# Performance work log

Hardware: AMD Instinct MI355X
Metric: run time of the kernel (lower is better)

The kernel has to match this reference:

```python
import jax, jax.numpy as jnp
import numpy as np

H, D = 8, 16
HD = H * D
SCALE0 = float(1.0 / np.sqrt(D * 1))   # degree-0 dot-product scale (order m=1)
SCALE1 = float(1.0 / np.sqrt(D * 3))   # degree-1 dot-product scale (order m=3)
SHARED = float(np.sqrt(0.5))           # shared_scale = sqrt(1/2) for DOT_PROD + SHARED
NEG = -1e9


def _split_heads_q(x):  # (b,n,HD,m) -> (b,H,n,D,m)
    b, n, _, m = x.shape
    return x.reshape(b, n, H, D, m).transpose(0, 2, 1, 3, 4)


def _split_heads_k(x):  # (b,n,N,HD,m) -> (b,H,n,N,D,m)
    b, n, N, _, m = x.shape
    return x.reshape(b, n, N, H, D, m).transpose(0, 3, 1, 2, 4, 5)


def _augment_kv(k, v, feats, W_self, null_k, null_v):
    # attend_self: VNLinear self key/value; use_null_kv: learned null tokens.
    b, n = feats.shape[:2]
    m = feats.shape[-1]
    skv = jnp.einsum('oc,bncm->bnom', W_self, feats)          # (b,n,2HD,m)
    sk, sv = jnp.split(skv, 2, axis=-2)
    sk = _split_heads_q(sk)[:, :, :, None]                     # (b,H,n,1,D,m)
    sv = _split_heads_q(sv)[:, :, :, None]
    nk = jnp.broadcast_to(null_k[None, :, None, None], (b, H, n, 1, D, m))
    nv = jnp.broadcast_to(null_v[None, :, None, None], (b, H, n, 1, D, m))
    k = jnp.concatenate([nk, sk, k], axis=3)                   # (b,H,n,2+N,D,m)
    v = jnp.concatenate([nv, sv, v], axis=3)
    return k, v


def _merge_heads(x):  # (b,H,n,D,m) -> (b,n,HD,m)
    b, _, n, _, m = x.shape
    return x.transpose(0, 2, 1, 3, 4).reshape(b, n, HD, m)


def _forward(q0, k0, v0, q1, k1, v1, feats0, feats1, edges,
             W_self_kv0, W_self_kv1, W_bias, self_bias, null_bias,
             null_k0, null_v0, null_k1, null_v1, head_weights1,
             W_out0, W_out1, neighbor_mask):
    b, n, N = edges.shape[:3]
    q0h, k0h, v0h = _split_heads_q(q0), _split_heads_k(k0), _split_heads_k(v0)
    q1h, k1h, v1h = _split_heads_q(q1), _split_heads_k(k1), _split_heads_k(v1)
    k0h, v0h = _augment_kv(k0h, v0h, feats0, W_self_kv0, null_k0, null_v0)
    k1h, v1h = _augment_kv(k1h, v1h, feats1, W_self_kv1, null_k1, null_v1)

    # pair bias for degree 0 (to_order==1); prepend null/self bias columns
    edge_bias = jnp.einsum('bnje,he->bhnj', edges, W_bias)     # (b,H,n,N)
    nb = jnp.broadcast_to(null_bias[None, :, None, None], (b, H, n, 1))
    sb = jnp.broadcast_to(self_bias[None, :, None, None], (b, H, n, 1))
    bias = jnp.concatenate([nb, sb, edge_bias], axis=-1)        # (b,H,n,2+N)

    sim0 = jnp.einsum('bhndm,bhnjdm->bhnj', q0h, k0h) * SCALE0 + bias
    w1 = jax.nn.softplus(head_weights1)                         # (1,H,1,1)
    sim1 = jnp.einsum('bhndm,bhnjdm->bhnj', q1h, k1h) * (SCALE1 * w1)

    total = (sim0 + sim1) * SHARED
    mask = jnp.concatenate(
        [jnp.ones((b, 1, n, 2), dtype=bool),                    # null + self always valid
         neighbor_mask[:, None]], axis=-1)
    total = jnp.where(mask, total, NEG)
    attn = jax.nn.softmax(total, axis=-1)                       # shared across degrees

    out0 = _merge_heads(jnp.einsum('bhnj,bhnjdm->bhndm', attn, v0h))
    out1 = _merge_heads(jnp.einsum('bhnj,bhnjdm->bhndm', attn, v1h))

    y0 = jnp.einsum('oc,bncm->bnom', W_out0, out0)              # FiberLinear deg 0
    y1 = jnp.einsum('oc,bncm->bnom', W_out1, out1)              # FiberLinear deg 1
    return y0, y1


def setup_inputs() -> dict:
    key = jax.random.key(0)
    ks = jax.random.split(key, 20)
    b, n, N, e = 1, 2048, 32, 32
    d0, d1 = 128, 64
    f = lambda k, s: jax.random.normal(k, s, dtype=jnp.float32) * 0.1
    return {
        'q0': f(ks[0], (b, n, HD, 1)), 'k0': f(ks[1], (b, n, N, HD, 1)), 'v0': f(ks[2], (b, n, N, HD, 1)),
        'q1': f(ks[3], (b, n, HD, 3)), 'k1': f(ks[4], (b, n, N, HD, 3)), 'v1': f(ks[5], (b, n, N, HD, 3)),
        'feats0': f(ks[6], (b, n, d0, 1)), 'feats1': f(ks[7], (b, n, d1, 3)),
        'edges': f(ks[8], (b, n, N, e)),
        'W_self_kv0': f(ks[9], (2 * HD, d0)), 'W_self_kv1': f(ks[10], (2 * HD, d1)),
        'W_bias': f(ks[11], (H, e)),
        'self_bias': jnp.zeros((H,), jnp.float32), 'null_bias': jnp.zeros((H,), jnp.float32),
        'null_k0': jnp.zeros((H, D, 1), jnp.float32), 'null_v0': jnp.zeros((H, D, 1), jnp.float32),
        'null_k1': jnp.zeros((H, D, 3), jnp.float32), 'null_v1': jnp.zeros((H, D, 3), jnp.float32),
        'head_weights1': jnp.full((1, H, 1, 1), float(np.log(np.e - 1.0)), jnp.float32),
        'W_out0': f(ks[12], (d0, HD)), 'W_out1': f(ks[13], (d1, HD)),
        'neighbor_mask': jax.random.uniform(ks[14], (b, n, N)) > 0.1,
    }


def reference(q0, k0, v0, q1, k1, v1, feats0, feats1, edges,
              W_self_kv0, W_self_kv1, W_bias, self_bias, null_bias,
              null_k0, null_v0, null_k1, null_v1, head_weights1,
              W_out0, W_out1, neighbor_mask):
    return _forward(q0, k0, v0, q1, k1, v1, feats0, feats1, edges,
                    W_self_kv0, W_self_kv1, W_bias, self_bias, null_bias,
                    null_k0, null_v0, null_k1, null_v1, head_weights1,
                    W_out0, W_out1, neighbor_mask)
```

## Files before the change

### kernel.cpp

```cpp
#include <hip/hip_runtime.h>

constexpr int kH  = 8;
constexpr int kD  = 16;
constexpr int kHD = 128;
constexpr int kN  = 32;
constexpr int kE  = 32;
constexpr int kD0 = 128;
constexpr int kD1 = 64;
constexpr int kP  = 4;
constexpr int kP3 = 2;

constexpr float SCALE0   = 0.25f;
constexpr float SCALE1   = 0.14433756729740643f;
constexpr float SHARED_S = 0.70710678118654752f;
constexpr float NEGV     = -1e9f;


__global__ __launch_bounds__(256) void k1_selfkv(
    const float* __restrict__ q0, const float* __restrict__ q1,
    const float* __restrict__ feats0, const float* __restrict__ feats1,
    const float* __restrict__ Wskv0, const float* __restrict__ Wskv1,
    const float* __restrict__ self_bias, const float* __restrict__ null_bias,
    const float* __restrict__ nk0, const float* __restrict__ nk1,
    const float* __restrict__ hw1,
    float* __restrict__ ws_sc, float* __restrict__ ws_sv0, float* __restrict__ ws_sv1)
{
  const int i0 = blockIdx.x * kP;
  const int t  = threadIdx.x;
  __shared__ __align__(16) float f0s[kP][kD0];
  __shared__ __align__(16) float f1s[kP][kD1 * 3];
  __shared__ __align__(16) float q0s[kP][kHD];
  __shared__ __align__(16) float q1s[kP][kHD * 3];
  __shared__ float sk0L[kP][kHD];
  __shared__ float sk1L[kP][kHD * 3];
  __shared__ float w1s[kH];

  for (int u = t; u < kP * 32; u += 256) { int p = u >> 5, r = u & 31;
    ((float4*)f0s[p])[r] = ((const float4*)(feats0 + (size_t)(i0 + p) * kD0))[r]; }
  for (int u = t; u < kP * 48; u += 256) { int p = u / 48, r = u % 48;
    ((float4*)f1s[p])[r] = ((const float4*)(feats1 + (size_t)(i0 + p) * kD1 * 3))[r]; }
  for (int u = t; u < kP * 32; u += 256) { int p = u >> 5, r = u & 31;
    ((float4*)q0s[p])[r] = ((const float4*)(q0 + (size_t)(i0 + p) * kHD))[r]; }
  for (int u = t; u < kP * 96; u += 256) { int p = u / 96, r = u % 96;
    ((float4*)q1s[p])[r] = ((const float4*)(q1 + (size_t)(i0 + p) * kHD * 3))[r]; }
  if (t < kH) w1s[t] = log1pf(expf(hw1[t]));
  __syncthreads();

  float acc0[kP] = {};
  {
    const float4* wr = (const float4*)(Wskv0 + t * kD0);
    #pragma unroll
    for (int g = 0; g < 32; ++g) {
      float4 w = wr[g]; int c = g * 4;
      #pragma unroll
      for (int p = 0; p < kP; ++p)
        acc0[p] += w.x * f0s[p][c] + w.y * f0s[p][c + 1]
                 + w.z * f0s[p][c + 2] + w.w * f0s[p][c + 3];
    }
  }
  float acc1[kP][3] = {};
  {
    const float4* wr = (const float4*)(Wskv1 + t * kD1);
    #pragma unroll
    for (int g = 0; g < 16; ++g) {
      float4 w = wr[g]; int c = g * 4;
      float wv[4] = {w.x, w.y, w.z, w.w};
      #pragma unroll
      for (int q = 0; q < 4; ++q) {
        #pragma unroll
        for (int p = 0; p < kP; ++p) {
          const float* fp = &f1s[p][(c + q) * 3];
          acc1[p][0] += wv[q] * fp[0];
          acc1[p][1] += wv[q] * fp[1];
          acc1[p][2] += wv[q] * fp[2];
        }
      }
    }
  }
  if (t < kHD) {
    #pragma unroll
    for (int p = 0; p < kP; ++p) {
      sk0L[p][t] = acc0[p];
      sk1L[p][t * 3 + 0] = acc1[p][0];
      sk1L[p][t * 3 + 1] = acc1[p][1];
      sk1L[p][t * 3 + 2] = acc1[p][2];
    }
  } else {
    const int o = t - kHD;
    #pragma unroll
    for (int p = 0; p < kP; ++p) {
      ws_sv0[(size_t)(i0 + p) * kHD + o] = acc0[p];
      float* sp = ws_sv1 + (size_t)(i0 + p) * kHD * 3 + o * 3;
      sp[0] = acc1[p][0]; sp[1] = acc1[p][1]; sp[2] = acc1[p][2];
    }
  }
  __syncthreads();

  if (t < kP * 16) {
    const int p = t >> 4, idx = t & 15;
    const int h = idx & 7;
    const bool is_self = idx >= 8;
    float s0 = 0.f, s1 = 0.f, bias;
    if (is_self) {
      #pragma unroll
      for (int d = 0; d < kD; ++d) s0 += q0s[p][h * kD + d] * sk0L[p][h * kD + d];
      #pragma unroll
      for (int x = 0; x < 48; ++x) s1 += q1s[p][h * 48 + x] * sk1L[p][h * 48 + x];
      bias = self_bias[h];
    } else {
      #pragma unroll
      for (int d = 0; d < kD; ++d) s0 += q0s[p][h * kD + d] * nk0[h * kD + d];
      #pragma unroll
      for (int x = 0; x < 48; ++x) s1 += q1s[p][h * 48 + x] * nk1[h * 48 + x];
      bias = null_bias[h];
    }
    float total = (s0 * SCALE0 + bias + s1 * SCALE1 * w1s[h]) * SHARED_S;
    ws_sc[(size_t)(i0 + p) * 272 + h * 34 + (is_self ? 1 : 0)] = total;
  }
}

__global__ __launch_bounds__(256) void k2_sims(
    const float* __restrict__ q0, const float* __restrict__ q1,
    const float* __restrict__ k0, const float* __restrict__ k1,
    const float* __restrict__ edges, const float* __restrict__ Wbias,
    const float* __restrict__ hw1, const int* __restrict__ nmask,
    float* __restrict__ ws_sc)
{
  const int i0 = blockIdx.x * kP;
  const int t  = threadIdx.x;
  __shared__ float q0s[kP][kH * 17];
  __shared__ float q1s[kP][kH * 49];
  __shared__ float edg[kP][kN * 33];
  __shared__ float wbT[kE * kH];
  __shared__ float w1s[kH];
  __shared__ __align__(16) float scL[kP][272];

  for (int u = t; u < kP * 32; u += 256) { int p = u >> 5, r = u & 31;
    float4 v = ((const float4*)(q0 + (size_t)(i0 + p) * kHD))[r];
    int c = r * 4, h = c >> 4, d = c & 15;
    float* dst = &q0s[p][h * 17 + d];
    dst[0] = v.x; dst[1] = v.y; dst[2] = v.z; dst[3] = v.w; }
  for (int u = t; u < kP * 96; u += 256) { int p = u / 96, r = u % 96;
    float4 v = ((const float4*)(q1 + (size_t)(i0 + p) * kHD * 3))[r];
    int c = r * 4, h = c / 48, x = c % 48;
    float* dst = &q1s[p][h * 49 + x];
    dst[0] = v.x; dst[1] = v.y; dst[2] = v.z; dst[3] = v.w; }
  for (int u = t; u < kP * 256; u += 256) { int p = u >> 8, r = u & 255;
    float4 v = ((const float4*)(edges + (size_t)(i0 + p) * kN * kE))[r];
    int j = r >> 3, e4 = (r & 7) * 4;
    float* dst = &edg[p][j * 33 + e4];
    dst[0] = v.x; dst[1] = v.y; dst[2] = v.z; dst[3] = v.w; }
  if (t < kH * kE) { int h = t >> 5, e = t & 31; wbT[e * 8 + h] = Wbias[t]; }
  if (t < kH) w1s[t] = log1pf(expf(hw1[t]));
  if (t < kP * 16) { int p = t >> 4, idx = t & 15, h = idx & 7, slot = idx >> 3;
    scL[p][h * 34 + slot] = ws_sc[(size_t)(i0 + p) * 272 + h * 34 + slot]; }
  __syncthreads();

  {
    const int j = t >> 3, h = t & 7;
    #pragma unroll
    for (int p = 0; p < kP; ++p) {
      const int i = i0 + p;
      float bias = 0.f;
      #pragma unroll
      for (int e = 0; e < kE; ++e) bias += edg[p][j * 33 + e] * wbT[e * 8 + h];
      float s0 = 0.f;
      const float4* kr0 = (const float4*)(k0 + (size_t)(i * kN + j) * kHD + h * kD);
      #pragma unroll
      for (int g = 0; g < 4; ++g) {
        float4 w = kr0[g]; int x = h * 17 + g * 4;
        s0 += w.x * q0s[p][x] + w.y * q0s[p][x + 1]
            + w.z * q0s[p][x + 2] + w.w * q0s[p][x + 3];
      }
      float s1 = 0.f;
      const float4* kr1 = (const float4*)(k1 + (size_t)(i * kN + j) * kHD * 3 + h * 48);
      #pragma unroll
      for (int g = 0; g < 12; ++g) {
        float4 w = kr1[g]; int x = h * 49 + g * 4;
        s1 += w.x * q1s[p][x] + w.y * q1s[p][x + 1]
            + w.z * q1s[p][x + 2] + w.w * q1s[p][x + 3];
      }
      float total = (s0 * SCALE0 + bias + s1 * SCALE1 * w1s[h]) * SHARED_S;
      bool valid = nmask[(size_t)i * kN + j] != 0;
      scL[p][h * 34 + 2 + j] = valid ? total : NEGV;
    }
  }
  __syncthreads();

  if (t < kP * kH) {
    const int p = t >> 3, h = t & 7;
    float* row = &scL[p][h * 34];
    float mx = -1e30f;
    #pragma unroll
    for (int u = 0; u < 34; ++u) mx = fmaxf(mx, row[u]);
    float sum = 0.f;
    #pragma unroll
    for (int u = 0; u < 34; ++u) sum += __expf(row[u] - mx);
    float inv = 1.f / sum;
    #pragma unroll
    for (int u = 0; u < 34; ++u) row[u] = __expf(row[u] - mx) * inv;
  }
  __syncthreads();

  for (int u = t; u < kP * 68; u += 256) {
    int p = u / 68, r = u % 68;
    ((float4*)(ws_sc + (size_t)(i0 + p) * 272))[r] = ((float4*)scL[p])[r];
  }
}

__global__ __launch_bounds__(256) void k3_out(
    const float* __restrict__ v0, const float* __restrict__ v1,
    const float* __restrict__ nv0, const float* __restrict__ nv1,
    const float* __restrict__ ws_sc,
    const float* __restrict__ ws_sv0, const float* __restrict__ ws_sv1,
    const float* __restrict__ Wout0, const float* __restrict__ Wout1,
    float* __restrict__ out, int n_total)
{
  const int i0 = blockIdx.x * kP3;
  const int t  = threadIdx.x;
  __shared__ __align__(16) float attnL[kP3][272];
  __shared__ __align__(16) float o0L[kP3][kHD];
  __shared__ __align__(16) float o1L[kP3][kHD * 3];

  if (t < kP3 * 68) {
    int p = t / 68, r = t % 68;
    ((float4*)attnL[p])[r] = ((const float4*)(ws_sc + (size_t)(i0 + p) * 272))[r];
  }
  __syncthreads();

  {
    const int p = t >> 7, i = i0 + p;
    const int s = t & 127;
    float4 acc;
    if (s < 32) {
      const int h = s >> 2;
      const float* at = attnL[p] + h * 34;
      float4 nv = ((const float4*)nv0)[s];
      float4 sv = ((const float4*)(ws_sv0 + (size_t)i * kHD))[s];
      acc.x = at[0] * nv.x + at[1] * sv.x;
      acc.y = at[0] * nv.y + at[1] * sv.y;
      acc.z = at[0] * nv.z + at[1] * sv.z;
      acc.w = at[0] * nv.w + at[1] * sv.w;
      const float4* vp = (const float4*)(v0 + (size_t)i * kN * kHD) + s;
      float4 vbuf[8];
      #pragma unroll
      for (int g = 0; g < 4; ++g) {
        #pragma unroll
        for (int r = 0; r < 8; ++r) vbuf[r] = vp[(g * 8 + r) * 32];
        #pragma unroll
        for (int r = 0; r < 8; ++r) {
          float a = at[2 + g * 8 + r];
          acc.x += a * vbuf[r].x; acc.y += a * vbuf[r].y;
          acc.z += a * vbuf[r].z; acc.w += a * vbuf[r].w;
        }
      }
      ((float4*)o0L[p])[s] = acc;
    } else {
      const int s1 = s - 32;
      const int h = s1 / 12;
      const float* at = attnL[p] + h * 34;
      float4 nv = ((const float4*)nv1)[s1];
      float4 sv = ((const float4*)(ws_sv1 + (size_t)i * kHD * 3))[s1];
      acc.x = at[0] * nv.x + at[1] * sv.x;
      acc.y = at[0] * nv.y + at[1] * sv.y;
      acc.z = at[0] * nv.z + at[1] * sv.z;
      acc.w = at[0] * nv.w + at[1] * sv.w;
      const float4* vp = (const float4*)(v1 + (size_t)i * kN * kHD * 3) + s1;
      float4 vbuf[8];
      #pragma unroll
      for (int g = 0; g < 4; ++g) {
        #pragma unroll
        for (int r = 0; r < 8; ++r) vbuf[r] = vp[(g * 8 + r) * 96];
        #pragma unroll
        for (int r = 0; r < 8; ++r) {
          float a = at[2 + g * 8 + r];
          acc.x += a * vbuf[r].x; acc.y += a * vbuf[r].y;
          acc.z += a * vbuf[r].z; acc.w += a * vbuf[r].w;
        }
      }
      ((float4*)o1L[p])[s1] = acc;
    }
  }
  __syncthreads();

  for (int u = t; u < 320; u += 256) {
    if (u < 128) {
      float acc[kP3] = {};
      const float4* wr = (const float4*)(Wout0 + u * kHD);
      #pragma unroll
      for (int g = 0; g < 32; ++g) {
        float4 w = wr[g]; int c = g * 4;
        #pragma unroll
        for (int p = 0; p < kP3; ++p)
          acc[p] += w.x * o0L[p][c] + w.y * o0L[p][c + 1]
                  + w.z * o0L[p][c + 2] + w.w * o0L[p][c + 3];
      }
      #pragma unroll
      for (int p = 0; p < kP3; ++p) out[(size_t)(i0 + p) * kHD + u] = acc[p];
    } else {
      const int v2 = u - 128, o = v2 / 3, m = v2 - o * 3;
      float acc[kP3] = {};
      const float4* wr = (const float4*)(Wout1 + o * kHD);
      #pragma unroll
      for (int g = 0; g < 32; ++g) {
        float4 w = wr[g]; int c = g * 4;
        #pragma unroll
        for (int p = 0; p < kP3; ++p)
          acc[p] += w.x * o1L[p][(c + 0) * 3 + m] + w.y * o1L[p][(c + 1) * 3 + m]
                  + w.z * o1L[p][(c + 2) * 3 + m] + w.w * o1L[p][(c + 3) * 3 + m];
      }
      #pragma unroll
      for (int p = 0; p < kP3; ++p)
        out[(size_t)n_total * kHD + (size_t)(i0 + p) * 192 + v2] = acc[p];
    }
  }
}

extern "C" void kernel_launch(void* const* d_in, const int* in_sizes, int n_in,
                              void* d_out, int out_size, void* d_ws, size_t ws_size,
                              hipStream_t stream) {
  const int n = in_sizes[0] / kHD;
  const float* q0     = (const float*)d_in[0];
  const float* k0     = (const float*)d_in[1];
  const float* v0     = (const float*)d_in[2];
  const float* q1     = (const float*)d_in[3];
  const float* k1     = (const float*)d_in[4];
  const float* v1     = (const float*)d_in[5];
  const float* feats0 = (const float*)d_in[6];
  const float* feats1 = (const float*)d_in[7];
  const float* edges  = (const float*)d_in[8];
  const float* Wskv0  = (const float*)d_in[9];
  const float* Wskv1  = (const float*)d_in[10];
  const float* Wbias  = (const float*)d_in[11];
  const float* sbias  = (const float*)d_in[12];
  const float* nbias  = (const float*)d_in[13];
  const float* nk0    = (const float*)d_in[14];
  const float* nv0    = (const float*)d_in[15];
  const float* nk1    = (const float*)d_in[16];
  const float* nv1    = (const float*)d_in[17];
  const float* hw1    = (const float*)d_in[18];
  const float* Wout0  = (const float*)d_in[19];
  const float* Wout1  = (const float*)d_in[20];
  const int*   nmask  = (const int*)d_in[21];

  float* ws     = (float*)d_ws;
  float* ws_sc  = ws;
  float* ws_sv0 = ws + (size_t)n * 272;
  float* ws_sv1 = ws + (size_t)n * 272 + (size_t)n * 128;

  k1_selfkv<<<n / kP, 256, 0, stream>>>(q0, q1, feats0, feats1, Wskv0, Wskv1,
                                        sbias, nbias, nk0, nk1, hw1,
                                        ws_sc, ws_sv0, ws_sv1);
  k2_sims<<<n / kP, 256, 0, stream>>>(q0, q1, k0, k1, edges, Wbias, hw1, nmask, ws_sc);
  k3_out<<<n / kP3, 256, 0, stream>>>(v0, v1, nv0, nv1, ws_sc, ws_sv0, ws_sv1,
                                      Wout0, Wout1, (float*)d_out, n);
}
```

Before: 372.3 us.

## Split output stage into accumulation kernel and batched projection kernel

The fused attention-accumulate plus output-projection kernel is split in two. The accumulation kernel writes the per-node attended values back into the self-value workspace buffers in place, with a launch-bounds occupancy hint. A new projection kernel loads eight nodes per block so each Wout row is reused across more nodes, replacing the previous two-node reuse. This adds a kernel launch and a round trip of the intermediate through global memory, and it underuses threads in the projection stage.

```diff
diff --git a/kernel.cpp b/kernel.cpp
--- a/kernel.cpp
+++ b/kernel.cpp
@@ -9,6 +9,7 @@
 constexpr int kD1 = 64;
 constexpr int kP  = 4;
 constexpr int kP3 = 2;
+constexpr int kPP = 8;
 
 constexpr float SCALE0   = 0.25f;
 constexpr float SCALE1   = 0.14433756729740643f;
@@ -208,19 +209,15 @@
   }
 }
 
-__global__ __launch_bounds__(256) void k3_out(
+__global__ __launch_bounds__(256, 4) void k3_accum(
     const float* __restrict__ v0, const float* __restrict__ v1,
     const float* __restrict__ nv0, const float* __restrict__ nv1,
     const float* __restrict__ ws_sc,
-    const float* __restrict__ ws_sv0, const float* __restrict__ ws_sv1,
-    const float* __restrict__ Wout0, const float* __restrict__ Wout1,
-    float* __restrict__ out, int n_total)
+    float* __restrict__ ws_sv0, float* __restrict__ ws_sv1)
 {
   const int i0 = blockIdx.x * kP3;
   const int t  = threadIdx.x;
   __shared__ __align__(16) float attnL[kP3][272];
-  __shared__ __align__(16) float o0L[kP3][kHD];
-  __shared__ __align__(16) float o1L[kP3][kHD * 3];
 
   if (t < kP3 * 68) {
     int p = t / 68, r = t % 68;
@@ -228,91 +225,103 @@
   }
   __syncthreads();
 
-  {
-    const int p = t >> 7, i = i0 + p;
-    const int s = t & 127;
-    float4 acc;
-    if (s < 32) {
-      const int h = s >> 2;
-      const float* at = attnL[p] + h * 34;
-      float4 nv = ((const float4*)nv0)[s];
-      float4 sv = ((const float4*)(ws_sv0 + (size_t)i * kHD))[s];
-      acc.x = at[0] * nv.x + at[1] * sv.x;
-      acc.y = at[0] * nv.y + at[1] * sv.y;
-      acc.z = at[0] * nv.z + at[1] * sv.z;
-      acc.w = at[0] * nv.w + at[1] * sv.w;
-      const float4* vp = (const float4*)(v0 + (size_t)i * kN * kHD) + s;
-      float4 vbuf[8];
-      #pragma unroll
-      for (int g = 0; g < 4; ++g) {
-        #pragma unroll
-        for (int r = 0; r < 8; ++r) vbuf[r] = vp[(g * 8 + r) * 32];
-        #pragma unroll
-        for (int r = 0; r < 8; ++r) {
-          float a = at[2 + g * 8 + r];
-          acc.x += a * vbuf[r].x; acc.y += a * vbuf[r].y;
-          acc.z += a * vbuf[r].z; acc.w += a * vbuf[r].w;
-        }
-      }
-      ((float4*)o0L[p])[s] = acc;
-    } else {
-      const int s1 = s - 32;
-      const int h = s1 / 12;
-      const float* at = attnL[p] + h * 34;
-      float4 nv = ((const float4*)nv1)[s1];
-      float4 sv = ((const float4*)(ws_sv1 + (size_t)i * kHD * 3))[s1];
-      acc.x = at[0] * nv.x + at[1] * sv.x;
-      acc.y = at[0] * nv.y + at[1] * sv.y;
-      acc.z = at[0] * nv.z + at[1] * sv.z;
-      acc.w = at[0] * nv.w + at[1] * sv.w;
-      const float4* vp = (const float4*)(v1 + (size_t)i * kN * kHD * 3) + s1;
-      float4 vbuf[8];
-      #pragma unroll
-      for (int g = 0; g < 4; ++g) {
-        #pragma unroll
-        for (int r = 0; r < 8; ++r) vbuf[r] = vp[(g * 8 + r) * 96];
-        #pragma unroll
-        for (int r = 0; r < 8; ++r) {
-          float a = at[2 + g * 8 + r];
-          acc.x += a * vbuf[r].x; acc.y += a * vbuf[r].y;
-          acc.z += a * vbuf[r].z; acc.w += a * vbuf[r].w;
-        }
-      }
-      ((float4*)o1L[p])[s1] = acc;
-    }
-  }
-  __syncthreads();
-
-  for (int u = t; u < 320; u += 256) {
-    if (u < 128) {
-      float acc[kP3] = {};
-      const float4* wr = (const float4*)(Wout0 + u * kHD);
-      #pragma unroll
-      for (int g = 0; g < 32; ++g) {
-        float4 w = wr[g]; int c = g * 4;
-        #pragma unroll
-        for (int p = 0; p < kP3; ++p)
-          acc[p] += w.x * o0L[p][c] + w.y * o0L[p][c + 1]
-                  + w.z * o0L[p][c + 2] + w.w * o0L[p][c + 3];
-      }
-      #pragma unroll
-      for (int p = 0; p < kP3; ++p) out[(size_t)(i0 + p) * kHD + u] = acc[p];
-    } else {
-      const int v2 = u - 128, o = v2 / 3, m = v2 - o * 3;
-      float acc[kP3] = {};
-      const float4* wr = (const float4*)(Wout1 + o * kHD);
-      #pragma unroll
-      for (int g = 0; g < 32; ++g) {
-        float4 w = wr[g]; int c = g * 4;
-        #pragma unroll
-        for (int p = 0; p < kP3; ++p)
-          acc[p] += w.x * o1L[p][(c + 0) * 3 + m] + w.y * o1L[p][(c + 1) * 3 + m]
-                  + w.z * o1L[p][(c + 2) * 3 + m] + w.w * o1L[p][(c + 3) * 3 + m];
-      }
-      #pragma unroll
-      for (int p = 0; p < kP3; ++p)
-        out[(size_t)n_total * kHD + (size_t)(i0 + p) * 192 + v2] = acc[p];
-    }
+  const int p = t >> 7, i = i0 + p;
+  const int s = t & 127;
+  float4 acc;
+  if (s < 32) {
+    const int h = s >> 2;
+    const float* at = attnL[p] + h * 34;
+    float4 nv = ((const float4*)nv0)[s];
+    float4 sv = ((const float4*)(ws_sv0 + (size_t)i * kHD))[s];
+    acc.x = at[0] * nv.x + at[1] * sv.x;
+    acc.y = at[0] * nv.y + at[1] * sv.y;
+    acc.z = at[0] * nv.z + at[1] * sv.z;
+    acc.w = at[0] * nv.w + at[1] * sv.w;
+    const float4* vp = (const float4*)(v0 + (size_t)i * kN * kHD) + s;
+    float4 vbuf[8];
+    #pragma unroll
+    for (int g = 0; g < 4; ++g) {
+      #pragma unroll
+      for (int r = 0; r < 8; ++r) vbuf[r] = vp[(g * 8 + r) * 32];
+      #pragma unroll
+      for (int r = 0; r < 8; ++r) {
+        float a = at[2 + g * 8 + r];
+        acc.x += a * vbuf[r].x; acc.y += a * vbuf[r].y;
+        acc.z += a * vbuf[r].z; acc.w += a * vbuf[r].w;
+      }
+    }
+    ((float4*)(ws_sv0 + (size_t)i * kHD))[s] = acc;
+  } else {
+    const int s1 = s - 32;
+    const int h = s1 / 12;
+    const float* at = attnL[p] + h * 34;
+    float4 nv = ((const float4*)nv1)[s1];
+    float4 sv = ((const float4*)(ws_sv1 + (size_t)i * kHD * 3))[s1];
+    acc.x = at[0] * nv.x + at[1] * sv.x;
+    acc.y = at[0] * nv.y + at[1] * sv.y;
+    acc.z = at[0] * nv.z + at[1] * sv.z;
+    acc.w = at[0] * nv.w + at[1] * sv.w;
+    const float4* vp = (const float4*)(v1 + (size_t)i * kN * kHD * 3) + s1;
+    float4 vbuf[8];
+    #pragma unroll
+    for (int g = 0; g < 4; ++g) {
+      #pragma unroll
+      for (int r = 0; r < 8; ++r) vbuf[r] = vp[(g * 8 + r) * 96];
+      #pragma unroll
+      for (int r = 0; r < 8; ++r) {
+        float a = at[2 + g * 8 + r];
+        acc.x += a * vbuf[r].x; acc.y += a * vbuf[r].y;
+        acc.z += a * vbuf[r].z; acc.w += a * vbuf[r].w;
+      }
+    }
+    ((float4*)(ws_sv1 + (size_t)i * kHD * 3))[s1] = acc;
+  }
+}
+
+__global__ __launch_bounds__(320) void k4_proj(
+    const float* __restrict__ ws_o0, const float* __restrict__ ws_o1,
+    const float* __restrict__ Wout0, const float* __restrict__ Wout1,
+    float* __restrict__ out, int n_total)
+{
+  const int i0 = blockIdx.x * kPP;
+  const int t  = threadIdx.x;
+  __shared__ __align__(16) float o0L[kPP][kHD];
+  __shared__ __align__(16) float o1L[kPP][kHD * 3];
+
+  for (int u = t; u < kPP * 32; u += 320) { int p = u >> 5, r = u & 31;
+    ((float4*)o0L[p])[r] = ((const float4*)(ws_o0 + (size_t)(i0 + p) * kHD))[r]; }
+  for (int u = t; u < kPP * 96; u += 320) { int p = u / 96, r = u % 96;
+    ((float4*)o1L[p])[r] = ((const float4*)(ws_o1 + (size_t)(i0 + p) * kHD * 3))[r]; }
+  __syncthreads();
+
+  if (t < 128) {
+    float acc[kPP] = {};
+    const float4* wr = (const float4*)(Wout0 + t * kHD);
+    #pragma unroll
+    for (int g = 0; g < 32; ++g) {
+      float4 w = wr[g]; int c = g * 4;
+      #pragma unroll
+      for (int p = 0; p < kPP; ++p)
+        acc[p] += w.x * o0L[p][c] + w.y * o0L[p][c + 1]
+                + w.z * o0L[p][c + 2] + w.w * o0L[p][c + 3];
+    }
+    #pragma unroll
+    for (int p = 0; p < kPP; ++p) out[(size_t)(i0 + p) * kHD + t] = acc[p];
+  } else {
+    const int v2 = t - 128, o = v2 / 3, m = v2 - o * 3;
+    float acc[kPP] = {};
+    const float4* wr = (const float4*)(Wout1 + o * kHD);
+    #pragma unroll
+    for (int g = 0; g < 32; ++g) {
+      float4 w = wr[g]; int c = g * 4;
+      #pragma unroll
+      for (int p = 0; p < kPP; ++p)
+        acc[p] += w.x * o1L[p][(c + 0) * 3 + m] + w.y * o1L[p][(c + 1) * 3 + m]
+                + w.z * o1L[p][(c + 2) * 3 + m] + w.w * o1L[p][(c + 3) * 3 + m];
+    }
+    #pragma unroll
+    for (int p = 0; p < kPP; ++p)
+      out[(size_t)n_total * kHD + (size_t)(i0 + p) * 192 + v2] = acc[p];
   }
 }
 
@@ -352,6 +361,6 @@
                                         sbias, nbias, nk0, nk1, hw1,
                                         ws_sc, ws_sv0, ws_sv1);
   k2_sims<<<n / kP, 256, 0, stream>>>(q0, q1, k0, k1, edges, Wbias, hw1, nmask, ws_sc);
-  k3_out<<<n / kP3, 256, 0, stream>>>(v0, v1, nv0, nv1, ws_sc, ws_sv0, ws_sv1,
-                                      Wout0, Wout1, (float*)d_out, n);
-}
+  k3_accum<<<n / kP3, 256, 0, stream>>>(v0, v1, nv0, nv1, ws_sc, ws_sv0, ws_sv1);
+  k4_proj<<<n / kPP, 320, 0, stream>>>(ws_sv0, ws_sv1, Wout0, Wout1, (float*)d_out, n);
+}
```

Measured after the change: 360.5 us. 1.03x faster.

## Fuse self-KV, similarity, softmax and output kernels into one kernel

Applied to the files above, without the earlier changes.

Merges the three kernels into a single kernel that processes two positions per block. Self key/value projections, scores and attention weights now stay in shared memory instead of going through a workspace. The GEMV-style loops are split across quads of lanes and combined with shuffle reductions, and the per-row softmax uses 16-lane shuffles. This removes two launches and the workspace round trips, but weight matrices are now re-read per two positions rather than four, and shared-memory use per block rises.

```diff
diff --git a/kernel.cpp b/kernel.cpp
--- a/kernel.cpp
+++ b/kernel.cpp
@@ -7,224 +7,230 @@
 constexpr int kE  = 32;
 constexpr int kD0 = 128;
 constexpr int kD1 = 64;
-constexpr int kP  = 4;
-constexpr int kP3 = 2;
+constexpr int kPos = 2;
 
 constexpr float SCALE0   = 0.25f;
 constexpr float SCALE1   = 0.14433756729740643f;
 constexpr float SHARED_S = 0.70710678118654752f;
 constexpr float NEGV     = -1e9f;
 
-
-__global__ __launch_bounds__(256) void k1_selfkv(
+__global__ __launch_bounds__(256, 4) void se3_fused(
     const float* __restrict__ q0, const float* __restrict__ q1,
+    const float* __restrict__ k0, const float* __restrict__ k1,
+    const float* __restrict__ v0, const float* __restrict__ v1,
     const float* __restrict__ feats0, const float* __restrict__ feats1,
+    const float* __restrict__ edges,
     const float* __restrict__ Wskv0, const float* __restrict__ Wskv1,
-    const float* __restrict__ self_bias, const float* __restrict__ null_bias,
+    const float* __restrict__ Wbias,
+    const float* __restrict__ sbias, const float* __restrict__ nbias,
     const float* __restrict__ nk0, const float* __restrict__ nk1,
+    const float* __restrict__ nv0, const float* __restrict__ nv1,
     const float* __restrict__ hw1,
-    float* __restrict__ ws_sc, float* __restrict__ ws_sv0, float* __restrict__ ws_sv1)
+    const float* __restrict__ Wout0, const float* __restrict__ Wout1,
+    const int* __restrict__ nmask,
+    float* __restrict__ out, int n_total)
 {
-  const int i0 = blockIdx.x * kP;
+  const int i0 = blockIdx.x * kPos;
   const int t  = threadIdx.x;
-  __shared__ __align__(16) float f0s[kP][kD0];
-  __shared__ __align__(16) float f1s[kP][kD1 * 3];
-  __shared__ __align__(16) float q0s[kP][kHD];
-  __shared__ __align__(16) float q1s[kP][kHD * 3];
-  __shared__ float sk0L[kP][kHD];
-  __shared__ float sk1L[kP][kHD * 3];
+
+  __shared__ __align__(16) float f0s[kPos][kD0];
+  __shared__ __align__(16) float f1s[kPos][kD1 * 3];
+  __shared__ __align__(16) float q0s[kPos][kHD];
+  __shared__ __align__(16) float q1s[kPos][kHD * 3];
+  __shared__ float edg[kPos][kN * (kE + 1)];
+  __shared__ float wbs[kH * kE];
   __shared__ float w1s[kH];
-
-  for (int u = t; u < kP * 32; u += 256) { int p = u >> 5, r = u & 31;
+  __shared__ int   nmL[kPos][kN];
+  __shared__ float sk0[kPos][kHD];
+  __shared__ __align__(16) float sk1[kPos][kHD * 3];
+  __shared__ __align__(16) float sv0[kPos][kHD];
+  __shared__ __align__(16) float sv1[kPos][kHD * 3];
+  __shared__ float sc[kPos][kH][36];
+  __shared__ __align__(16) float o0[kPos][kHD];
+  __shared__ __align__(16) float o1[kPos][kHD * 3];
+
+  if (t < kPos * 32) { int p = t >> 5, r = t & 31;
     ((float4*)f0s[p])[r] = ((const float4*)(feats0 + (size_t)(i0 + p) * kD0))[r]; }
-  for (int u = t; u < kP * 48; u += 256) { int p = u / 48, r = u % 48;
+  else if (t < kPos * 32 + kPos * 48) { int u = t - kPos * 32, p = u / 48, r = u % 48;
     ((float4*)f1s[p])[r] = ((const float4*)(feats1 + (size_t)(i0 + p) * kD1 * 3))[r]; }
-  for (int u = t; u < kP * 32; u += 256) { int p = u >> 5, r = u & 31;
+  if (t >= 160 && t < 160 + kPos * 32) { int u = t - 160, p = u >> 5, r = u & 31;
     ((float4*)q0s[p])[r] = ((const float4*)(q0 + (size_t)(i0 + p) * kHD))[r]; }
-  for (int u = t; u < kP * 96; u += 256) { int p = u / 96, r = u % 96;
-    ((float4*)q1s[p])[r] = ((const float4*)(q1 + (size_t)(i0 + p) * kHD * 3))[r]; }
+  {
+    int u = t; if (u < kPos * 96) { int p = u / 96, r = u % 96;
+      ((float4*)q1s[p])[r] = ((const float4*)(q1 + (size_t)(i0 + p) * kHD * 3))[r]; }
+  }
+  for (int u = t; u < kPos * 256; u += 256) { int p = u >> 8, r = u & 255;
+    float4 v = ((const float4*)(edges + (size_t)(i0 + p) * kN * kE))[r];
+    int j = r >> 3, e4 = (r & 7) * 4;
+    float* dst = &edg[p][j * 33 + e4];
+    dst[0] = v.x; dst[1] = v.y; dst[2] = v.z; dst[3] = v.w; }
+  if (t < kH * kE) wbs[t] = Wbias[t];
   if (t < kH) w1s[t] = log1pf(expf(hw1[t]));
-  __syncthreads();
-
-  float acc0[kP] = {};
-  {
-    const float4* wr = (const float4*)(Wskv0 + t * kD0);
-    #pragma unroll
-    for (int g = 0; g < 32; ++g) {
-      float4 w = wr[g]; int c = g * 4;
-      #pragma unroll
-      for (int p = 0; p < kP; ++p)
-        acc0[p] += w.x * f0s[p][c] + w.y * f0s[p][c + 1]
-                 + w.z * f0s[p][c + 2] + w.w * f0s[p][c + 3];
-    }
-  }
-  float acc1[kP][3] = {};
-  {
-    const float4* wr = (const float4*)(Wskv1 + t * kD1);
-    #pragma unroll
-    for (int g = 0; g < 16; ++g) {
-      float4 w = wr[g]; int c = g * 4;
+  if (t < kPos * kN) { int p = t >> 5, j = t & 31;
+    nmL[p][j] = nmask[(size_t)(i0 + p) * kN + j]; }
+  __syncthreads();
+
+  const int q4 = t & 3;
+  const int qg = t >> 2;
+
+  #pragma unroll
+  for (int pass = 0; pass < 4; ++pass) {
+    const int r = qg + 64 * pass;
+    const float4* w0r = (const float4*)(Wskv0 + (size_t)r * kD0);
+    float a0[kPos] = {};
+    #pragma unroll
+    for (int g = 0; g < 8; ++g) {
+      float4 w = w0r[q4 + 4 * g]; int c = (q4 + 4 * g) * 4;
+      #pragma unroll
+      for (int p = 0; p < kPos; ++p)
+        a0[p] += w.x * f0s[p][c] + w.y * f0s[p][c + 1]
+               + w.z * f0s[p][c + 2] + w.w * f0s[p][c + 3];
+    }
+    const float4* w1r = (const float4*)(Wskv1 + (size_t)r * kD1);
+    float a1[kPos][3] = {};
+    #pragma unroll
+    for (int g = 0; g < 4; ++g) {
+      float4 w = w1r[q4 + 4 * g]; int c = (q4 + 4 * g) * 4;
       float wv[4] = {w.x, w.y, w.z, w.w};
       #pragma unroll
-      for (int q = 0; q < 4; ++q) {
-        #pragma unroll
-        for (int p = 0; p < kP; ++p) {
-          const float* fp = &f1s[p][(c + q) * 3];
-          acc1[p][0] += wv[q] * fp[0];
-          acc1[p][1] += wv[q] * fp[1];
-          acc1[p][2] += wv[q] * fp[2];
-        }
-      }
-    }
-  }
-  if (t < kHD) {
-    #pragma unroll
-    for (int p = 0; p < kP; ++p) {
-      sk0L[p][t] = acc0[p];
-      sk1L[p][t * 3 + 0] = acc1[p][0];
-      sk1L[p][t * 3 + 1] = acc1[p][1];
-      sk1L[p][t * 3 + 2] = acc1[p][2];
-    }
-  } else {
-    const int o = t - kHD;
-    #pragma unroll
-    for (int p = 0; p < kP; ++p) {
-      ws_sv0[(size_t)(i0 + p) * kHD + o] = acc0[p];
-      float* sp = ws_sv1 + (size_t)(i0 + p) * kHD * 3 + o * 3;
-      sp[0] = acc1[p][0]; sp[1] = acc1[p][1]; sp[2] = acc1[p][2];
-    }
-  }
-  __syncthreads();
-
-  if (t < kP * 16) {
+      for (int k = 0; k < 4; ++k) {
+        #pragma unroll
+        for (int p = 0; p < kPos; ++p) {
+          const float* fp = &f1s[p][(c + k) * 3];
+          a1[p][0] += wv[k] * fp[0];
+          a1[p][1] += wv[k] * fp[1];
+          a1[p][2] += wv[k] * fp[2];
+        }
+      }
+    }
+    #pragma unroll
+    for (int p = 0; p < kPos; ++p) {
+      a0[p] += __shfl_xor(a0[p], 1); a0[p] += __shfl_xor(a0[p], 2);
+      #pragma unroll
+      for (int c = 0; c < 3; ++c) {
+        a1[p][c] += __shfl_xor(a1[p][c], 1);
+        a1[p][c] += __shfl_xor(a1[p][c], 2);
+      }
+    }
+    if (q4 == 0) {
+      if (r < kHD) {
+        #pragma unroll
+        for (int p = 0; p < kPos; ++p) {
+          sk0[p][r] = a0[p];
+          sk1[p][r * 3 + 0] = a1[p][0];
+          sk1[p][r * 3 + 1] = a1[p][1];
+          sk1[p][r * 3 + 2] = a1[p][2];
+        }
+      } else {
+        const int o = r - kHD;
+        #pragma unroll
+        for (int p = 0; p < kPos; ++p) {
+          sv0[p][o] = a0[p];
+          sv1[p][o * 3 + 0] = a1[p][0];
+          sv1[p][o * 3 + 1] = a1[p][1];
+          sv1[p][o * 3 + 2] = a1[p][2];
+        }
+      }
+    }
+  }
+  __syncthreads();
+
+  if (t < kPos * 16) {
     const int p = t >> 4, idx = t & 15;
     const int h = idx & 7;
     const bool is_self = idx >= 8;
     float s0 = 0.f, s1 = 0.f, bias;
     if (is_self) {
       #pragma unroll
-      for (int d = 0; d < kD; ++d) s0 += q0s[p][h * kD + d] * sk0L[p][h * kD + d];
-      #pragma unroll
-      for (int x = 0; x < 48; ++x) s1 += q1s[p][h * 48 + x] * sk1L[p][h * 48 + x];
-      bias = self_bias[h];
+      for (int d = 0; d < kD; ++d) s0 += q0s[p][h * kD + d] * sk0[p][h * kD + d];
+      #pragma unroll
+      for (int x = 0; x < 48; ++x) s1 += q1s[p][h * 48 + x] * sk1[p][h * 48 + x];
+      bias = sbias[h];
     } else {
       #pragma unroll
       for (int d = 0; d < kD; ++d) s0 += q0s[p][h * kD + d] * nk0[h * kD + d];
       #pragma unroll
       for (int x = 0; x < 48; ++x) s1 += q1s[p][h * 48 + x] * nk1[h * 48 + x];
-      bias = null_bias[h];
-    }
-    float total = (s0 * SCALE0 + bias + s1 * SCALE1 * w1s[h]) * SHARED_S;
-    ws_sc[(size_t)(i0 + p) * 272 + h * 34 + (is_self ? 1 : 0)] = total;
-  }
-}
-
-__global__ __launch_bounds__(256) void k2_sims(
-    const float* __restrict__ q0, const float* __restrict__ q1,
-    const float* __restrict__ k0, const float* __restrict__ k1,
-    const float* __restrict__ edges, const float* __restrict__ Wbias,
-    const float* __restrict__ hw1, const int* __restrict__ nmask,
-    float* __restrict__ ws_sc)
-{
-  const int i0 = blockIdx.x * kP;
-  const int t  = threadIdx.x;
-  __shared__ float q0s[kP][kH * 17];
-  __shared__ float q1s[kP][kH * 49];
-  __shared__ float edg[kP][kN * 33];
-  __shared__ float wbT[kE * kH];
-  __shared__ float w1s[kH];
-  __shared__ __align__(16) float scL[kP][272];
-
-  for (int u = t; u < kP * 32; u += 256) { int p = u >> 5, r = u & 31;
-    float4 v = ((const float4*)(q0 + (size_t)(i0 + p) * kHD))[r];
-    int c = r * 4, h = c >> 4, d = c & 15;
-    float* dst = &q0s[p][h * 17 + d];
-    dst[0] = v.x; dst[1] = v.y; dst[2] = v.z; dst[3] = v.w; }
-  for (int u = t; u < kP * 96; u += 256) { int p = u / 96, r = u % 96;
-    float4 v = ((const float4*)(q1 + (size_t)(i0 + p) * kHD * 3))[r];
-    int c = r * 4, h = c / 48, x = c % 48;
-    float* dst = &q1s[p][h * 49 + x];
-    dst[0] = v.x; dst[1] = v.y; dst[2] = v.z; dst[3] = v.w; }
-  for (int u = t; u < kP * 256; u += 256) { int p = u >> 8, r = u & 255;
-    float4 v = ((const float4*)(edges + (size_t)(i0 + p) * kN * kE))[r];
-    int j = r >> 3, e4 = (r & 7) * 4;
-    float* dst = &edg[p][j * 33 + e4];
-    dst[0] = v.x; dst[1] = v.y; dst[2] = v.z; dst[3] = v.w; }
-  if (t < kH * kE) { int h = t >> 5, e = t & 31; wbT[e * 8 + h] = Wbias[t]; }
-  if (t < kH) w1s[t] = log1pf(expf(hw1[t]));
-  if (t < kP * 16) { int p = t >> 4, idx = t & 15, h = idx & 7, slot = idx >> 3;
-    scL[p][h * 34 + slot] = ws_sc[(size_t)(i0 + p) * 272 + h * 34 + slot]; }
-  __syncthreads();
+      bias = nbias[h];
+    }
+    sc[p][h][is_self ? 1 : 0] =
+        (s0 * SCALE0 + bias + s1 * SCALE1 * w1s[h]) * SHARED_S;
+  }
 
   {
-    const int j = t >> 3, h = t & 7;
-    #pragma unroll
-    for (int p = 0; p < kP; ++p) {
+    const int h  = qg & 7;
+    const int jl = qg >> 3;
+    const float w1h = w1s[h];
+    float wbf[8];
+    #pragma unroll
+    for (int e = 0; e < 8; ++e) wbf[e] = wbs[h * kE + q4 * 8 + e];
+
+    #pragma unroll
+    for (int p = 0; p < kPos; ++p) {
       const int i = i0 + p;
-      float bias = 0.f;
-      #pragma unroll
-      for (int e = 0; e < kE; ++e) bias += edg[p][j * 33 + e] * wbT[e * 8 + h];
-      float s0 = 0.f;
-      const float4* kr0 = (const float4*)(k0 + (size_t)(i * kN + j) * kHD + h * kD);
-      #pragma unroll
-      for (int g = 0; g < 4; ++g) {
-        float4 w = kr0[g]; int x = h * 17 + g * 4;
-        s0 += w.x * q0s[p][x] + w.y * q0s[p][x + 1]
-            + w.z * q0s[p][x + 2] + w.w * q0s[p][x + 3];
-      }
-      float s1 = 0.f;
-      const float4* kr1 = (const float4*)(k1 + (size_t)(i * kN + j) * kHD * 3 + h * 48);
-      #pragma unroll
-      for (int g = 0; g < 12; ++g) {
-        float4 w = kr1[g]; int x = h * 49 + g * 4;
-        s1 += w.x * q1s[p][x] + w.y * q1s[p][x + 1]
-            + w.z * q1s[p][x + 2] + w.w * q1s[p][x + 3];
-      }
-      float total = (s0 * SCALE0 + bias + s1 * SCALE1 * w1s[h]) * SHARED_S;
-      bool valid = nmask[(size_t)i * kN + j] != 0;
-      scL[p][h * 34 + 2 + j] = valid ? total : NEGV;
-    }
-  }
-  __syncthreads();
-
-  if (t < kP * kH) {
-    const int p = t >> 3, h = t & 7;
-    float* row = &scL[p][h * 34];
-    float mx = -1e30f;
-    #pragma unroll
-    for (int u = 0; u < 34; ++u) mx = fmaxf(mx, row[u]);
-    float sum = 0.f;
-    #pragma unroll
-    for (int u = 0; u < 34; ++u) sum += __expf(row[u] - mx);
-    float inv = 1.f / sum;
-    #pragma unroll
-    for (int u = 0; u < 34; ++u) row[u] = __expf(row[u] - mx) * inv;
-  }
-  __syncthreads();
-
-  for (int u = t; u < kP * 68; u += 256) {
-    int p = u / 68, r = u % 68;
-    ((float4*)(ws_sc + (size_t)(i0 + p) * 272))[r] = ((float4*)scL[p])[r];
-  }
-}
-
-__global__ __launch_bounds__(256) void k3_out(
-    const float* __restrict__ v0, const float* __restrict__ v1,
-    const float* __restrict__ nv0, const float* __restrict__ nv1,
-    const float* __restrict__ ws_sc,
-    const float* __restrict__ ws_sv0, const float* __restrict__ ws_sv1,
-    const float* __restrict__ Wout0, const float* __restrict__ Wout1,
-    float* __restrict__ out, int n_total)
-{
-  const int i0 = blockIdx.x * kP3;
-  const int t  = threadIdx.x;
-  __shared__ __align__(16) float attnL[kP3][272];
-  __shared__ __align__(16) float o0L[kP3][kHD];
-  __shared__ __align__(16) float o1L[kP3][kHD * 3];
-
-  if (t < kP3 * 68) {
-    int p = t / 68, r = t % 68;
-    ((float4*)attnL[p])[r] = ((const float4*)(ws_sc + (size_t)(i0 + p) * 272))[r];
+      const float4 q0f = *((const float4*)(q0s[p] + h * kD) + q4);
+      float4 q1f[3];
+      #pragma unroll
+      for (int pc = 0; pc < 3; ++pc)
+        q1f[pc] = *((const float4*)(q1s[p] + h * 48 + pc * 16) + q4);
+
+      const float* k0base = k0 + (size_t)i * kN * kHD + h * kD + q4 * 4;
+      const float* k1base = k1 + (size_t)i * kN * kHD * 3 + h * 48 + q4 * 4;
+
+      float4 kv0[4];
+      float4 kv1[4][3];
+      #pragma unroll
+      for (int pp = 0; pp < 4; ++pp) {
+        const int j = pp * 8 + jl;
+        kv0[pp] = *((const float4*)(k0base + (size_t)j * kHD));
+        #pragma unroll
+        for (int pc = 0; pc < 3; ++pc)
+          kv1[pp][pc] = *((const float4*)(k1base + (size_t)j * kHD * 3 + pc * 16));
+      }
+
+      #pragma unroll
+      for (int pp = 0; pp < 4; ++pp) {
+        const int j = pp * 8 + jl;
+        float s0 = kv0[pp].x * q0f.x + kv0[pp].y * q0f.y
+                 + kv0[pp].z * q0f.z + kv0[pp].w * q0f.w;
+        float s1 = 0.f;
+        #pragma unroll
+        for (int pc = 0; pc < 3; ++pc)
+          s1 += kv1[pp][pc].x * q1f[pc].x + kv1[pp][pc].y * q1f[pc].y
+              + kv1[pp][pc].z * q1f[pc].z + kv1[pp][pc].w * q1f[pc].w;
+        float bias = 0.f;
+        #pragma unroll
+        for (int e = 0; e < 8; ++e) bias += edg[p][j * 33 + q4 * 8 + e] * wbf[e];
+
+        float part = s0 * SCALE0 + bias + s1 * SCALE1 * w1h;
+        part += __shfl_xor(part, 1);
+        part += __shfl_xor(part, 2);
+        if (q4 == 0) sc[p][h][2 + j] = nmL[p][j] ? part * SHARED_S : NEGV;
+      }
+    }
+  }
+  __syncthreads();
+
+  {
+    const int row = t >> 4;
+    const int p = row >> 3, h = row & 7, l = t & 15;
+    float* rp = sc[p][h];
+    float va = rp[2 + l], vb = rp[2 + l + 16];
+    float mx = fmaxf(va, vb);
+    #pragma unroll
+    for (int off = 8; off > 0; off >>= 1) mx = fmaxf(mx, __shfl_xor(mx, off));
+    float e0v = rp[0], e1v = rp[1];
+    mx = fmaxf(mx, fmaxf(e0v, e1v));
+    float ea = __expf(va - mx), eb = __expf(vb - mx);
+    float sum = ea + eb;
+    #pragma unroll
+    for (int off = 8; off > 0; off >>= 1) sum += __shfl_xor(sum, off);
+    float ee0 = __expf(e0v - mx), ee1 = __expf(e1v - mx);
+    float inv = 1.f / (sum + ee0 + ee1);
+    rp[2 + l] = ea * inv;
+    rp[2 + l + 16] = eb * inv;
+    if (l == 0) rp[0] = ee0 * inv;
+    if (l == 1) rp[1] = ee1 * inv;
   }
   __syncthreads();
 
@@ -234,9 +240,9 @@
     float4 acc;
     if (s < 32) {
       const int h = s >> 2;
-      const float* at = attnL[p] + h * 34;
+      const float* at = sc[p][h];
       float4 nv = ((const float4*)nv0)[s];
-      float4 sv = ((const float4*)(ws_sv0 + (size_t)i * kHD))[s];
+      float4 sv = ((const float4*)sv0[p])[s];
       acc.x = at[0] * nv.x + at[1] * sv.x;
       acc.y = at[0] * nv.y + at[1] * sv.y;
       acc.z = at[0] * nv.z + at[1] * sv.z;
@@ -254,13 +260,13 @@
           acc.z += a * vbuf[r].z; acc.w += a * vbuf[r].w;
         }
       }
-      ((float4*)o0L[p])[s] = acc;
+      ((float4*)o0[p])[s] = acc;
     } else {
       const int s1 = s - 32;
       const int h = s1 / 12;
-      const float* at = attnL[p] + h * 34;
+      const float* at = sc[p][h];
       float4 nv = ((const float4*)nv1)[s1];
-      float4 sv = ((const float4*)(ws_sv1 + (size_t)i * kHD * 3))[s1];
+      float4 sv = ((const float4*)sv1[p])[s1];
       acc.x = at[0] * nv.x + at[1] * sv.x;
       acc.y = at[0] * nv.y + at[1] * sv.y;
       acc.z = at[0] * nv.z + at[1] * sv.z;
@@ -278,40 +284,55 @@
           acc.z += a * vbuf[r].z; acc.w += a * vbuf[r].w;
         }
       }
-      ((float4*)o1L[p])[s1] = acc;
-    }
-  }
-  __syncthreads();
-
-  for (int u = t; u < 320; u += 256) {
+      ((float4*)o1[p])[s1] = acc;
+    }
+  }
+  __syncthreads();
+
+  #pragma unroll
+  for (int pass = 0; pass < 5; ++pass) {
+    const int u = qg + 64 * pass;
     if (u < 128) {
-      float acc[kP3] = {};
-      const float4* wr = (const float4*)(Wout0 + u * kHD);
-      #pragma unroll
-      for (int g = 0; g < 32; ++g) {
-        float4 w = wr[g]; int c = g * 4;
-        #pragma unroll
-        for (int p = 0; p < kP3; ++p)
-          acc[p] += w.x * o0L[p][c] + w.y * o0L[p][c + 1]
-                  + w.z * o0L[p][c + 2] + w.w * o0L[p][c + 3];
-      }
-      #pragma unroll
-      for (int p = 0; p < kP3; ++p) out[(size_t)(i0 + p) * kHD + u] = acc[p];
+      const float4* wr = (const float4*)(Wout0 + (size_t)u * kHD);
+      float a[kPos] = {};
+      #pragma unroll
+      for (int g = 0; g < 8; ++g) {
+        float4 w = wr[q4 + 4 * g]; int c = (q4 + 4 * g) * 4;
+        #pragma unroll
+        for (int p = 0; p < kPos; ++p)
+          a[p] += w.x * o0[p][c] + w.y * o0[p][c + 1]
+                + w.z * o0[p][c + 2] + w.w * o0[p][c + 3];
+      }
+      #pragma unroll
+      for (int p = 0; p < kPos; ++p) {
+        a[p] += __shfl_xor(a[p], 1); a[p] += __shfl_xor(a[p], 2);
+      }
+      if (q4 == 0) {
+        #pragma unroll
+        for (int p = 0; p < kPos; ++p)
+          out[(size_t)(i0 + p) * kHD + u] = a[p];
+      }
     } else {
       const int v2 = u - 128, o = v2 / 3, m = v2 - o * 3;
-      float acc[kP3] = {};
-      const float4* wr = (const float4*)(Wout1 + o * kHD);
-      #pragma unroll
-      for (int g = 0; g < 32; ++g) {
-        float4 w = wr[g]; int c = g * 4;
-        #pragma unroll
-        for (int p = 0; p < kP3; ++p)
-          acc[p] += w.x * o1L[p][(c + 0) * 3 + m] + w.y * o1L[p][(c + 1) * 3 + m]
-                  + w.z * o1L[p][(c + 2) * 3 + m] + w.w * o1L[p][(c + 3) * 3 + m];
-      }
-      #pragma unroll
-      for (int p = 0; p < kP3; ++p)
-        out[(size_t)n_total * kHD + (size_t)(i0 + p) * 192 + v2] = acc[p];
+      const float4* wr = (const float4*)(Wout1 + (size_t)o * kHD);
+      float a[kPos] = {};
+      #pragma unroll
+      for (int g = 0; g < 8; ++g) {
+        float4 w = wr[q4 + 4 * g]; int c = (q4 + 4 * g) * 4;
+        #pragma unroll
+        for (int p = 0; p < kPos; ++p)
+          a[p] += w.x * o1[p][(c + 0) * 3 + m] + w.y * o1[p][(c + 1) * 3 + m]
+                + w.z * o1[p][(c + 2) * 3 + m] + w.w * o1[p][(c + 3) * 3 + m];
+      }
+      #pragma unroll
+      for (int p = 0; p < kPos; ++p) {
+        a[p] += __shfl_xor(a[p], 1); a[p] += __shfl_xor(a[p], 2);
+      }
+      if (q4 == 0) {
+        #pragma unroll
+        for (int p = 0; p < kPos; ++p)
+          out[(size_t)n_total * kHD + (size_t)(i0 + p) * 192 + v2] = a[p];
+      }
     }
   }
 }
@@ -343,15 +364,8 @@
   const float* Wout1  = (const float*)d_in[20];
   const int*   nmask  = (const int*)d_in[21];
 
-  float* ws     = (float*)d_ws;
-  float* ws_sc  = ws;
-  float* ws_sv0 = ws + (size_t)n * 272;
-  float* ws_sv1 = ws + (size_t)n * 272 + (size_t)n * 128;
-
-  k1_selfkv<<<n / kP, 256, 0, stream>>>(q0, q1, feats0, feats1, Wskv0, Wskv1,
-                                        sbias, nbias, nk0, nk1, hw1,
-                                        ws_sc, ws_sv0, ws_sv1);
-  k2_sims<<<n / kP, 256, 0, stream>>>(q0, q1, k0, k1, edges, Wbias, hw1, nmask, ws_sc);
-  k3_out<<<n / kP3, 256, 0, stream>>>(v0, v1, nv0, nv1, ws_sc, ws_sv0, ws_sv1,
-                                      Wout0, Wout1, (float*)d_out, n);
+  se3_fused<<<n / kPos, 256, 0, stream>>>(
+      q0, q1, k0, k1, v0, v1, feats0, feats1, edges,
+      Wskv0, Wskv1, Wbias, sbias, nbias, nk0, nk1, nv0, nv1, hw1,
+      Wout0, Wout1, nmask, (float*)d_out, n);
 }
```

Measured after the change: 324.6 us. 1.15x faster.
